# Optimization experiments

Hardware: AMD Instinct MI355X
Metric: run time of the kernel (lower is better)

Reference implementation:

```python
import jax, jax.numpy as jnp
import numpy as np

B, S, D = 8, 1024, 1024
H, K = 16, 64  # num_heads, key_dim
NEG_INF = -1e9  # Keras _large_compatible_negative for float32


def setup_inputs() -> dict:
    key = jax.random.key(0)
    ks = jax.random.split(key, 10)
    x = jax.random.normal(ks[0], (B, S, D), dtype=jnp.float32)
    mask = jax.random.bernoulli(ks[1], 0.9, (B, S))  # bool per-token mask
    w = lambda k, shp: (0.02 * jax.random.normal(k, shp, dtype=jnp.float32))
    return {
        "input_tensor": x,
        "input_mask": mask,
        "Wq": w(ks[2], (D, H, K)), "bq": jnp.zeros((H, K), jnp.float32),
        "Wk": w(ks[3], (D, H, K)), "bk": jnp.zeros((H, K), jnp.float32),
        "Wv": w(ks[4], (D, H, K)), "bv": jnp.zeros((H, K), jnp.float32),
        "Wo": w(ks[5], (H, K, D)), "bo": jnp.zeros((D,), jnp.float32),
    }


def reference(input_tensor, input_mask, Wq, bq, Wk, bk, Wv, bv, Wo, bo):
    x = input_tensor
    # QKV projections: [B,S,D] x [D,H,K] -> [B,S,H,K]
    q = jnp.einsum("bsd,dhk->bshk", x, Wq) + bq
    k = jnp.einsum("bsd,dhk->bshk", x, Wk) + bk
    v = jnp.einsum("bsd,dhk->bshk", x, Wv) + bv
    # scaled dot-product scores: [B,H,Sq,Sk]
    scores = jnp.einsum("bqhk,bshk->bhqs", q, k) / jnp.sqrt(
        jnp.asarray(K, x.dtype))
    # mask = logical_and(mask[...,None], mask[...,None,:]) per example
    m2 = (input_mask[:, :, None] & input_mask[:, None, :])  # [B,Sq,Sk]
    scores = scores + (1.0 - m2[:, None, :, :].astype(x.dtype)) * NEG_INF
    probs = jax.nn.softmax(scores, axis=-1)
    # attend and project out: [B,S,H,K] -> [B,S,D]
    ctx = jnp.einsum("bhqs,bshk->bqhk", probs, v)
    return jnp.einsum("bqhk,hkd->bqd", ctx, Wo) + bo
```

## Files before the change

kernel.cpp:

```cpp
#include <hip/hip_runtime.h>
#include <math.h>

#define Ss 1024
#define Dd 1024
#define Hh 16
#define Kk 64

typedef __bf16 bf16x8 __attribute__((ext_vector_type(8)));
typedef __bf16 bf16x4 __attribute__((ext_vector_type(4)));
typedef float  f32x4  __attribute__((ext_vector_type(4)));

#define MFMA16(a, b, c) __builtin_amdgcn_mfma_f32_16x16x32_bf16(a, b, c, 0, 0, 0)

#define XB_E   8388608u
#define WT_E   3145728u
#define WOT_E  1048576u
#define QKV_E  8388608u

#define QSC 0.18033688011112042f

__device__ __forceinline__ float exp2_hw(float x) {
    float r; asm("v_exp_f32 %0, %1" : "=v"(r) : "v"(x)); return r;
}

typedef __attribute__((address_space(1))) const void gas_void;
typedef __attribute__((address_space(3))) void las_void;
__device__ __forceinline__ void gll16(const __bf16* g, char* l) {
    __builtin_amdgcn_global_load_lds((gas_void*)g, (las_void*)l, 16, 0, 0);
}

__global__ __launch_bounds__(256) void prep(
    const float* __restrict__ x,
    const float* __restrict__ Wq, const float* __restrict__ Wk,
    const float* __restrict__ Wv, const float* __restrict__ Wo,
    __bf16* __restrict__ xb, __bf16* __restrict__ WT, __bf16* __restrict__ WoT)
{
    __shared__ float tile[64][65];
    const int z = blockIdx.z;
    const int t = threadIdx.x;

    if (z == 4) {
        size_t blk = blockIdx.y * 16 + blockIdx.x;
        const float4* src = (const float4*)(x + blk * 32768);
        bf16x4* dst = (bf16x4*)(((__bf16*)xb) + blk * 32768);
        #pragma unroll
        for (int u = 0; u < 32; ++u) {
            float4 v = src[u * 256 + t];
            dst[u * 256 + t] =
                (bf16x4){(__bf16)v.x, (__bf16)v.y, (__bf16)v.z, (__bf16)v.w};
        }
        return;
    }

    const float* src = (z == 0) ? Wq : (z == 1) ? Wk : (z == 2) ? Wv : Wo;
    __bf16* dst = (z < 3) ? (WT + (size_t)z * 1048576) : WoT;

    int r0 = blockIdx.y * 64, c0 = blockIdx.x * 64;
    int rr = t >> 2, cg = (t & 3) * 16;

    #pragma unroll
    for (int u = 0; u < 4; ++u) {
        float4 v = *(const float4*)(src + (size_t)(r0 + rr) * 1024 + c0 + cg + u * 4);
        tile[rr][cg + u * 4 + 0] = v.x;
        tile[rr][cg + u * 4 + 1] = v.y;
        tile[rr][cg + u * 4 + 2] = v.z;
        tile[rr][cg + u * 4 + 3] = v.w;
    }
    __syncthreads();
    bf16x8 o0, o1;
    #pragma unroll
    for (int jj = 0; jj < 8; ++jj) o0[jj] = (__bf16)tile[cg + jj][rr];
    #pragma unroll
    for (int jj = 0; jj < 8; ++jj) o1[jj] = (__bf16)tile[cg + 8 + jj][rr];
    __bf16* dp = dst + (size_t)(c0 + rr) * 1024 + r0 + cg;
    *(bf16x8*)dp = o0;
    *(bf16x8*)(dp + 8) = o1;
}

__global__ __launch_bounds__(512, 2) void gemm_qkv(
    const __bf16* __restrict__ A, const __bf16* __restrict__ Bt,
    __bf16* __restrict__ qb, __bf16* __restrict__ kb, __bf16* __restrict__ vb,
    const float* __restrict__ bq, const float* __restrict__ bk,
    const float* __restrict__ bv)
{
    __shared__ __align__(16) __bf16 As[2][256][64];
    __shared__ __align__(16) __bf16 Bs[2][256][64];

    const int t = threadIdx.x;
    const int wave = t >> 6, lane = t & 63;
    const int quad = lane >> 4, l16 = lane & 15;
    const int wm = wave >> 2, wn = wave & 3;

    const int nwg = gridDim.x * gridDim.y;
    const int cpx = nwg >> 3;
    int g = blockIdx.y * gridDim.x + blockIdx.x;
    g = (g & 7) * cpx + (g >> 3);
    const int bx = g % gridDim.x, by = g / gridDim.x;
    const int m0 = by * 256, n0 = bx * 256;

    const int srow = t >> 3;
    const int scol = (((t & 7) ^ (srow & 7)) * 8);
    const __bf16* pa = A  + (size_t)(m0 + srow) * 1024 + scol;
    const __bf16* pb = Bt + (size_t)(n0 + srow) * 1024 + scol;
    char* lA = (char*)(&As[0][0][0]) + t * 16;
    char* lB = (char*)(&Bs[0][0][0]) + t * 16;

#define STAGE(slot, k0) do {                                     \
        gll16(pa + (k0),           lA + (slot) * 32768);         \
        gll16(pa + (k0) +  65536,  lA + (slot) * 32768 +  8192); \
        gll16(pa + (k0) + 131072,  lA + (slot) * 32768 + 16384); \
        gll16(pa + (k0) + 196608,  lA + (slot) * 32768 + 24576); \
        gll16(pb + (k0),           lB + (slot) * 32768);         \
        gll16(pb + (k0) +  65536,  lB + (slot) * 32768 +  8192); \
        gll16(pb + (k0) + 131072,  lB + (slot) * 32768 + 16384); \
        gll16(pb + (k0) + 196608,  lB + (slot) * 32768 + 24576); \
    } while (0)

    STAGE(0, 0);
    STAGE(1, 64);

    f32x4 acc[8][4];
    #pragma unroll
    for (int i = 0; i < 8; ++i)
        #pragma unroll
        for (int j = 0; j < 4; ++j) acc[i][j] = (f32x4){0.f, 0.f, 0.f, 0.f};

    const int swz = (l16 & 7) << 4;

    for (int it = 0; it < 16; ++it) {
        const int s = it & 1;
        if (it == 15) asm volatile("s_waitcnt vmcnt(0)" ::: "memory");
        else          asm volatile("s_waitcnt vmcnt(8)" ::: "memory");
        __builtin_amdgcn_s_barrier();

        const char* baseA = (const char*)&As[s][0][0];
        const char* baseB = (const char*)&Bs[s][0][0];

        bf16x8 bfrag[2][4];
        #pragma unroll
        for (int nj = 0; nj < 4; ++nj) {
            int rowb = (wn * 64 + nj * 16 + l16) * 128;
            bfrag[0][nj] = *(const bf16x8*)(baseB + rowb + ((quad * 16) ^ swz));
            bfrag[1][nj] = *(const bf16x8*)(baseB + rowb + ((64 + quad * 16) ^ swz));
        }

        {
            bf16x8 afr[4][2];
            #pragma unroll
            for (int mi = 0; mi < 4; ++mi) {
                int rowa = (wm * 128 + mi * 16 + l16) * 128;
                afr[mi][0] = *(const bf16x8*)(baseA + rowa + ((quad * 16) ^ swz));
                afr[mi][1] = *(const bf16x8*)(baseA + rowa + ((64 + quad * 16) ^ swz));
            }
            __builtin_amdgcn_s_setprio(1);
            #pragma unroll
            for (int mi = 0; mi < 4; ++mi)
                #pragma unroll
                for (int nj = 0; nj < 4; ++nj)
                    acc[mi][nj] = MFMA16(afr[mi][1], bfrag[1][nj],
                                  MFMA16(afr[mi][0], bfrag[0][nj], acc[mi][nj]));
            __builtin_amdgcn_s_setprio(0);
        }
        __builtin_amdgcn_s_barrier();

        {
            bf16x8 afr[4][2];
            #pragma unroll
            for (int mi = 0; mi < 4; ++mi) {
                int rowa = (wm * 128 + (mi + 4) * 16 + l16) * 128;
                afr[mi][0] = *(const bf16x8*)(baseA + rowa + ((quad * 16) ^ swz));
                afr[mi][1] = *(const bf16x8*)(baseA + rowa + ((64 + quad * 16) ^ swz));
            }
            asm volatile("s_waitcnt lgkmcnt(0)" ::: "memory");
            __builtin_amdgcn_sched_barrier(0);
            __builtin_amdgcn_s_barrier();
            if (it < 14) STAGE(s, (it + 2) * 64);

            __builtin_amdgcn_s_setprio(1);
            #pragma unroll
            for (int mi = 0; mi < 4; ++mi)
                #pragma unroll
                for (int nj = 0; nj < 4; ++nj)
                    acc[mi + 4][nj] = MFMA16(afr[mi][1], bfrag[1][nj],
                                      MFMA16(afr[mi][0], bfrag[0][nj], acc[mi + 4][nj]));
            __builtin_amdgcn_s_setprio(0);
        }
    }
#undef STAGE

    {
        const int z = n0 >> 10;
        const float* bias = (z == 0) ? bq : (z == 1) ? bk : bv;
        const float sc2 = (z == 0) ? QSC : 1.0f;
        #pragma unroll
        for (int mi = 0; mi < 8; ++mi) {
            int row = m0 + wm * 128 + mi * 16 + quad * 4;
            int b = row >> 10, sx = row & 1023;
            #pragma unroll
            for (int nj = 0; nj < 4; ++nj) {
                int n1 = (n0 + wn * 64 + nj * 16 + l16) & 1023;
                int h = n1 >> 6, ch = n1 & 63;
                float bia = bias[n1];
                if (z < 2) {
                    __bf16* dst = ((z == 0) ? qb : kb)
                        + ((size_t)(b * Hh + h) * Ss + sx) * Kk + ch;
                    #pragma unroll
                    for (int r = 0; r < 4; ++r)
                        dst[(size_t)r * Kk] = (__bf16)((acc[mi][nj][r] + bia) * sc2);
                } else {
                    float bia2 = bv[n1];
                    bf16x4 o;
                    #pragma unroll
                    for (int r = 0; r < 4; ++r) o[r] = (__bf16)(acc[mi][nj][r] + bia2);
                    *(bf16x4*)(vb + ((size_t)(b * Hh + h) * Kk + ch) * Ss + sx) = o;
                }
            }
        }
    }
}

__global__ __launch_bounds__(512) void gemm_out(
    const __bf16* __restrict__ A, const __bf16* __restrict__ Bt,
    float* __restrict__ outf, const float* __restrict__ bo)
{
    __shared__ __align__(16) __bf16 As[2][256][64];
    __shared__ __align__(16) __bf16 Bs[2][128][64];

    const int t = threadIdx.x;
    const int wave = t >> 6, lane = t & 63;
    const int quad = lane >> 4, l16 = lane & 15;
    const int wm = wave >> 2, wn = wave & 3;

    const int nwg = gridDim.x * gridDim.y;
    const int cpx = nwg >> 3;
    int g = blockIdx.y * gridDim.x + blockIdx.x;
    g = (g & 7) * cpx + (g >> 3);
    const int bx = g % gridDim.x, by = g / gridDim.x;
    const int m0 = by * 256, n0 = bx * 128;

    const int srow = t >> 3;
    const int scol = (((t & 7) ^ (srow & 7)) * 8);
    const __bf16* pa = A  + (size_t)(m0 + srow) * 1024 + scol;
    const __bf16* pb = Bt + (size_t)(n0 + srow) * 1024 + scol;
    char* lA = (char*)(&As[0][0][0]) + t * 16;
    char* lB = (char*)(&Bs[0][0][0]) + t * 16;

#define SGA(slot, k0, c) gll16(pa + (k0) + (c) * 65536, lA + (slot) * 32768 + (c) * 8192)
#define SGB(slot, k0, c) gll16(pb + (k0) + (c) * 65536, lB + (slot) * 16384 + (c) * 8192)

    SGA(0, 0, 0); SGA(0, 0, 2);
    SGB(0, 0, 0); SGB(0, 0, 1);
    SGA(0, 0, 1); SGA(0, 0, 3);

    f32x4 acc[8][2];
    #pragma unroll
    for (int i = 0; i < 8; ++i)
        #pragma unroll
        for (int j = 0; j < 2; ++j) acc[i][j] = (f32x4){0.f, 0.f, 0.f, 0.f};

    const int swz = (l16 & 7) << 4;

    asm volatile("s_waitcnt vmcnt(2)" ::: "memory");
    __syncthreads();

    for (int it = 0; it < 16; ++it) {
        const int s = it & 1, ns = s ^ 1;
        const int kn = (it + 1) * 64;
        const bool st = (it < 15);
        const char* baseA = (const char*)&As[s][0][0];
        const char* baseB = (const char*)&Bs[s][0][0];

        bf16x8 af[4][2], b0f[2][2];

        asm volatile("s_waitcnt vmcnt(0)" ::: "memory");
        #pragma unroll
        for (int mi = 0; mi < 4; ++mi) {
            int ra = (wm * 128 + mi * 16 + l16) * 128;
            af[mi][0] = *(const bf16x8*)(baseA + ra + ((quad * 16) ^ swz));
            af[mi][1] = *(const bf16x8*)(baseA + ra + ((64 + quad * 16) ^ swz));
        }
        #pragma unroll
        for (int nj = 0; nj < 2; ++nj) {
            int rb = (wn * 32 + nj * 16 + l16) * 128;
            b0f[nj][0] = *(const bf16x8*)(baseB + rb + ((quad * 16) ^ swz));
            b0f[nj][1] = *(const bf16x8*)(baseB + rb + ((64 + quad * 16) ^ swz));
        }
        if (st) { SGA(ns, kn, 0); SGA(ns, kn, 2); SGB(ns, kn, 0); SGB(ns, kn, 1); }
        __builtin_amdgcn_s_barrier();
        asm volatile("s_waitcnt lgkmcnt(0)" ::: "memory");
        __builtin_amdgcn_sched_barrier(0);
        __builtin_amdgcn_s_setprio(1);
        #pragma unroll
        for (int mi = 0; mi < 4; ++mi)
            #pragma unroll
            for (int nj = 0; nj < 2; ++nj)
                acc[mi][nj] = MFMA16(af[mi][1], b0f[nj][1],
                              MFMA16(af[mi][0], b0f[nj][0], acc[mi][nj]));
        __builtin_amdgcn_s_setprio(0);
        __builtin_amdgcn_s_barrier();

        asm volatile("s_waitcnt vmcnt(0)" ::: "memory");
        #pragma unroll
        for (int mi = 0; mi < 4; ++mi) {
            int ra = (wm * 128 + (4 + mi) * 16 + l16) * 128;
            af[mi][0] = *(const bf16x8*)(baseA + ra + ((quad * 16) ^ swz));
            af[mi][1] = *(const bf16x8*)(baseA + ra + ((64 + quad * 16) ^ swz));
        }
        if (st) { SGA(ns, kn, 1); SGA(ns, kn, 3); }
        __builtin_amdgcn_s_barrier();
        asm volatile("s_waitcnt lgkmcnt(0)" ::: "memory");
        __builtin_amdgcn_sched_barrier(0);
        __builtin_amdgcn_s_setprio(1);
        #pragma unroll
        for (int mi = 0; mi < 4; ++mi)
            #pragma unroll
            for (int nj = 0; nj < 2; ++nj)
                acc[4 + mi][nj] = MFMA16(af[mi][1], b0f[nj][1],
                                  MFMA16(af[mi][0], b0f[nj][0], acc[4 + mi][nj]));
        __builtin_amdgcn_s_setprio(0);
        __builtin_amdgcn_s_barrier();
    }
#undef SGA
#undef SGB

    #pragma unroll
    for (int mi = 0; mi < 8; ++mi) {
        int row = m0 + wm * 128 + mi * 16 + quad * 4;
        #pragma unroll
        for (int nj = 0; nj < 2; ++nj) {
            int n = n0 + wn * 32 + nj * 16 + l16;
            float bia = bo[n];
            #pragma unroll
            for (int r = 0; r < 4; ++r)
                outf[(size_t)(row + r) * 1024 + n] = acc[mi][nj][r] + bia;
        }
    }
}

__global__ __launch_bounds__(256) void attn(
    const __bf16* __restrict__ qb, const __bf16* __restrict__ kb,
    const __bf16* __restrict__ vb, const int* __restrict__ mask,
    __bf16* __restrict__ ctx)
{
    const int id = blockIdx.y * gridDim.x + blockIdx.x;
    const int bh = (id & 7) * 16 + ((id >> 3) & 15);
    const int q0 = (id >> 7) * 128;
    const int b  = bh >> 4;
    const int h  = bh & 15;
    const size_t base = (size_t)bh * Ss * Kk;

    __shared__ __align__(16) __bf16 Qs[128][72];
    __shared__ __align__(16) __bf16 Ks[2][64][72];
    __shared__ __align__(16) __bf16 VTs[2][64][72];
    __shared__ __align__(16) __bf16 Ps[4][32][72];
    __shared__ float mkf[1024];

    const int t    = threadIdx.x;
    const int wave = t >> 6, lane = t & 63;
    const int quad = lane >> 4, l16 = lane & 15;
    const int qbase = wave * 32;

    #pragma unroll
    for (int p = 0; p < 4; ++p) {
        int idx = t + p * 256;
        int r = idx >> 3, gq = idx & 7;
        *(bf16x8*)&Qs[r][gq * 8] =
            *(const bf16x8*)(qb + base + (size_t)(q0 + r) * Kk + gq * 8);
    }
    {
        int4 mi = *(const int4*)(mask + b * Ss + t * 4);
        mkf[t * 4 + 0] = (float)mi.x;
        mkf[t * 4 + 1] = (float)mi.y;
        mkf[t * 4 + 2] = (float)mi.z;
        mkf[t * 4 + 3] = (float)mi.w;
    }

    const int r0 = t >> 3, c0 = (t & 7) * 8;
    bf16x8 kr0, kr1, vr0, vr1;
    kr0 = *(const bf16x8*)(kb + base + (size_t)(r0) * Kk + c0);
    kr1 = *(const bf16x8*)(kb + base + (size_t)(r0 + 32) * Kk + c0);
    vr0 = *(const bf16x8*)(vb + base + (size_t)(r0) * Ss + c0);
    vr1 = *(const bf16x8*)(vb + base + (size_t)(r0 + 32) * Ss + c0);

    __syncthreads();

    bf16x8 aq[2][2];
    #pragma unroll
    for (int rg = 0; rg < 2; ++rg) {
        aq[rg][0] = *(const bf16x8*)&Qs[qbase + rg * 16 + l16][quad * 8];
        aq[rg][1] = *(const bf16x8*)&Qs[qbase + rg * 16 + l16][32 + quad * 8];
    }
    float mqf[2][4], omqf[2][4];
    #pragma unroll
    for (int rg = 0; rg < 2; ++rg)
        #pragma unroll
        for (int i = 0; i < 4; ++i) {
            float m = mkf[q0 + qbase + rg * 16 + quad * 4 + i];
            mqf[rg][i] = m; omqf[rg][i] = 1.0f - m;
        }

    f32x4 O[2][4];
    float lsum[2][4];
    #pragma unroll
    for (int rg = 0; rg < 2; ++rg)
        #pragma unroll
        for (int nb = 0; nb < 4; ++nb) O[rg][nb] = (f32x4){0.f, 0.f, 0.f, 0.f};
    #pragma unroll
    for (int rg = 0; rg < 2; ++rg)
        #pragma unroll
        for (int i = 0; i < 4; ++i) lsum[rg][i] = 0.f;

    for (int kt = 0; kt < Ss; kt += 64) {
        const int p = (kt >> 6) & 1;
        *(bf16x8*)&Ks[p][r0][c0] = kr0;
        *(bf16x8*)&Ks[p][r0 + 32][c0] = kr1;
        *(bf16x8*)&VTs[p][r0][c0] = vr0;
        *(bf16x8*)&VTs[p][r0 + 32][c0] = vr1;
        __syncthreads();

        int ktn = kt + 64;
        if (ktn < Ss) {
            kr0 = *(const bf16x8*)(kb + base + (size_t)(ktn + r0) * Kk + c0);
            kr1 = *(const bf16x8*)(kb + base + (size_t)(ktn + r0 + 32) * Kk + c0);
            vr0 = *(const bf16x8*)(vb + base + (size_t)(r0) * Ss + ktn + c0);
            vr1 = *(const bf16x8*)(vb + base + (size_t)(r0 + 32) * Ss + ktn + c0);
        }

        float mkv[4];
        #pragma unroll
        for (int nb = 0; nb < 4; ++nb) mkv[nb] = mkf[kt + nb * 16 + l16];

        bf16x8 kb0[4], kb1[4];
        #pragma unroll
        for (int nb = 0; nb < 4; ++nb) {
            kb0[nb] = *(const bf16x8*)&Ks[p][nb * 16 + l16][quad * 8];
            kb1[nb] = *(const bf16x8*)&Ks[p][nb * 16 + l16][32 + quad * 8];
        }

        f32x4 s[2][4];
        __builtin_amdgcn_s_setprio(1);
        #pragma unroll
        for (int rg = 0; rg < 2; ++rg)
            #pragma unroll
            for (int nb = 0; nb < 4; ++nb) {
                f32x4 a = (f32x4){0.f, 0.f, 0.f, 0.f};
                a = MFMA16(aq[rg][0], kb0[nb], a);
                a = MFMA16(aq[rg][1], kb1[nb], a);
                s[rg][nb] = a;
            }
        __builtin_amdgcn_s_setprio(0);

        #pragma unroll
        for (int rg = 0; rg < 2; ++rg)
            #pragma unroll
            for (int i = 0; i < 4; ++i) {
                float ls = 0.f;
                #pragma unroll
                for (int nb = 0; nb < 4; ++nb) {
                    float pv = exp2_hw(s[rg][nb][i]) * mkv[nb];
                    pv = pv * mqf[rg][i] + omqf[rg][i];
                    Ps[wave][rg * 16 + quad * 4 + i][nb * 16 + l16] = (__bf16)pv;
                    ls += pv;
                }
                lsum[rg][i] += ls;
            }

        bf16x8 ap0[2], ap1[2];
        #pragma unroll
        for (int rg = 0; rg < 2; ++rg) {
            ap0[rg] = *(const bf16x8*)&Ps[wave][rg * 16 + l16][quad * 8];
            ap1[rg] = *(const bf16x8*)&Ps[wave][rg * 16 + l16][32 + quad * 8];
        }
        __builtin_amdgcn_s_setprio(1);
        #pragma unroll
        for (int nb = 0; nb < 4; ++nb) {
            bf16x8 vb0 = *(const bf16x8*)&VTs[p][nb * 16 + l16][quad * 8];
            bf16x8 vb1 = *(const bf16x8*)&VTs[p][nb * 16 + l16][32 + quad * 8];
            #pragma unroll
            for (int rg = 0; rg < 2; ++rg) {
                O[rg][nb] = MFMA16(ap0[rg], vb0, O[rg][nb]);
                O[rg][nb] = MFMA16(ap1[rg], vb1, O[rg][nb]);
            }
        }
        __builtin_amdgcn_s_setprio(0);
    }

    #pragma unroll
    for (int rg = 0; rg < 2; ++rg)
        #pragma unroll
        for (int i = 0; i < 4; ++i) {
            float l = lsum[rg][i];
            l += __shfl_xor(l, 1);
            l += __shfl_xor(l, 2);
            l += __shfl_xor(l, 4);
            l += __shfl_xor(l, 8);
            float inv = 1.0f / l;
            int srow = q0 + qbase + rg * 16 + quad * 4 + i;
            __bf16* dst = ctx + ((size_t)(b * Ss + srow) * Hh + h) * Kk;
            #pragma unroll
            for (int nb = 0; nb < 4; ++nb)
                dst[nb * 16 + l16] = (__bf16)(O[rg][nb][i] * inv);
        }
}

extern "C" void kernel_launch(void* const* d_in, const int* in_sizes, int n_in,
                              void* d_out, int out_size, void* d_ws, size_t ws_size,
                              hipStream_t stream) {
    const float* x    = (const float*)d_in[0];
    const int*   mask = (const int*)d_in[1];
    const float* Wq   = (const float*)d_in[2];
    const float* bq   = (const float*)d_in[3];
    const float* Wk   = (const float*)d_in[4];
    const float* bk   = (const float*)d_in[5];
    const float* Wv   = (const float*)d_in[6];
    const float* bv   = (const float*)d_in[7];
    const float* Wo   = (const float*)d_in[8];
    const float* bo   = (const float*)d_in[9];

    __bf16* xb   = (__bf16*)d_ws;
    __bf16* WT   = xb + XB_E;
    __bf16* WoT  = WT + WT_E;
    __bf16* qb   = WoT + WOT_E;
    __bf16* kb   = qb + QKV_E;
    __bf16* vb   = kb + QKV_E;
    __bf16* ctxb = vb + QKV_E;
    float* out = (float*)d_out;

    prep<<<dim3(16, 16, 5), 256, 0, stream>>>(x, Wq, Wk, Wv, Wo, xb, WT, WoT);
    gemm_qkv<<<dim3(12, 32), 512, 0, stream>>>(xb, WT, qb, kb, vb, bq, bk, bv);
    attn<<<dim3(128, 8), 256, 0, stream>>>(qb, kb, vb, mask, ctxb);
    gemm_out<<<dim3(8, 32), 512, 0, stream>>>(ctxb, WoT, out, bo);
}
```

Baseline: 259.8 us.

## Compute transposed scores and shuffle P in registers to drop LDS staging

The attention kernel now computes S^T (K as the A operand), so each lane holds one query row's scores. The probabilities are packed to bf16 with v_cvt_pk and rearranged into the PV MFMA operand with cross-lane shuffles, which removes the Ps shared-memory round trip. Q fragments are loaded straight from global memory, so the Qs tile is gone and LDS use drops, and launch bounds request 3 blocks per SIMD. The block index mapping is simplified and the output is written as vectorized bf16x4 stores. In exchange each tile now runs many shuffles, and the occupancy hint adds register pressure.

```diff
diff --git a/kernel.cpp b/kernel.cpp
--- a/kernel.cpp
+++ b/kernel.cpp
@@ -21,6 +21,11 @@
 
 __device__ __forceinline__ float exp2_hw(float x) {
     float r; asm("v_exp_f32 %0, %1" : "=v"(r) : "v"(x)); return r;
+}
+__device__ __forceinline__ unsigned cvtpk(float lo, float hi) {
+    unsigned r;
+    asm("v_cvt_pk_bf16_f32 %0, %1, %2" : "=v"(r) : "v"(lo), "v"(hi));
+    return r;
 }
 
 typedef __attribute__((address_space(1))) const void gas_void;
@@ -337,22 +342,19 @@
     }
 }
 
-__global__ __launch_bounds__(256) void attn(
+__global__ __launch_bounds__(256, 3) void attn(
     const __bf16* __restrict__ qb, const __bf16* __restrict__ kb,
     const __bf16* __restrict__ vb, const int* __restrict__ mask,
     __bf16* __restrict__ ctx)
 {
-    const int id = blockIdx.y * gridDim.x + blockIdx.x;
-    const int bh = (id & 7) * 16 + ((id >> 3) & 15);
-    const int q0 = (id >> 7) * 128;
+    const int bh = blockIdx.x;
+    const int q0 = blockIdx.y * 128;
     const int b  = bh >> 4;
     const int h  = bh & 15;
     const size_t base = (size_t)bh * Ss * Kk;
 
-    __shared__ __align__(16) __bf16 Qs[128][72];
     __shared__ __align__(16) __bf16 Ks[2][64][72];
     __shared__ __align__(16) __bf16 VTs[2][64][72];
-    __shared__ __align__(16) __bf16 Ps[4][32][72];
     __shared__ float mkf[1024];
 
     const int t    = threadIdx.x;
@@ -360,13 +362,6 @@
     const int quad = lane >> 4, l16 = lane & 15;
     const int qbase = wave * 32;
 
-    #pragma unroll
-    for (int p = 0; p < 4; ++p) {
-        int idx = t + p * 256;
-        int r = idx >> 3, gq = idx & 7;
-        *(bf16x8*)&Qs[r][gq * 8] =
-            *(const bf16x8*)(qb + base + (size_t)(q0 + r) * Kk + gq * 8);
-    }
     {
         int4 mi = *(const int4*)(mask + b * Ss + t * 4);
         mkf[t * 4 + 0] = (float)mi.x;
@@ -382,33 +377,33 @@
     vr0 = *(const bf16x8*)(vb + base + (size_t)(r0) * Ss + c0);
     vr1 = *(const bf16x8*)(vb + base + (size_t)(r0 + 32) * Ss + c0);
 
+    bf16x8 aq[2][2];
+    #pragma unroll
+    for (int rg = 0; rg < 2; ++rg) {
+        const __bf16* qrow = qb + base + (size_t)(q0 + qbase + rg * 16 + l16) * Kk;
+        aq[rg][0] = *(const bf16x8*)(qrow + quad * 8);
+        aq[rg][1] = *(const bf16x8*)(qrow + 32 + quad * 8);
+    }
+
     __syncthreads();
 
-    bf16x8 aq[2][2];
+    float mq[2], omq[2];
     #pragma unroll
     for (int rg = 0; rg < 2; ++rg) {
-        aq[rg][0] = *(const bf16x8*)&Qs[qbase + rg * 16 + l16][quad * 8];
-        aq[rg][1] = *(const bf16x8*)&Qs[qbase + rg * 16 + l16][32 + quad * 8];
-    }
-    float mqf[2][4], omqf[2][4];
+        float m_ = mkf[q0 + qbase + rg * 16 + l16];
+        mq[rg] = m_; omq[rg] = 1.0f - m_;
+    }
+
+    f32x4 O[2][4];
+    float lsum[2] = {0.f, 0.f};
     #pragma unroll
     for (int rg = 0; rg < 2; ++rg)
         #pragma unroll
-        for (int i = 0; i < 4; ++i) {
-            float m = mkf[q0 + qbase + rg * 16 + quad * 4 + i];
-            mqf[rg][i] = m; omqf[rg][i] = 1.0f - m;
-        }
-
-    f32x4 O[2][4];
-    float lsum[2][4];
-    #pragma unroll
-    for (int rg = 0; rg < 2; ++rg)
-        #pragma unroll
         for (int nb = 0; nb < 4; ++nb) O[rg][nb] = (f32x4){0.f, 0.f, 0.f, 0.f};
-    #pragma unroll
-    for (int rg = 0; rg < 2; ++rg)
-        #pragma unroll
-        for (int i = 0; i < 4; ++i) lsum[rg][i] = 0.f;
+
+    const int SA = ((quad & 1) << 5) | l16;
+    const int SB = SA + 16;
+    const bool hi = (quad >> 1) != 0;
 
     for (int kt = 0; kt < Ss; kt += 64) {
         const int p = (kt >> 6) & 1;
@@ -426,10 +421,6 @@
             vr1 = *(const bf16x8*)(vb + base + (size_t)(r0 + 32) * Ss + ktn + c0);
         }
 
-        float mkv[4];
-        #pragma unroll
-        for (int nb = 0; nb < 4; ++nb) mkv[nb] = mkf[kt + nb * 16 + l16];
-
         bf16x8 kb0[4], kb1[4];
         #pragma unroll
         for (int nb = 0; nb < 4; ++nb) {
@@ -444,63 +435,78 @@
             #pragma unroll
             for (int nb = 0; nb < 4; ++nb) {
                 f32x4 a = (f32x4){0.f, 0.f, 0.f, 0.f};
-                a = MFMA16(aq[rg][0], kb0[nb], a);
-                a = MFMA16(aq[rg][1], kb1[nb], a);
+                a = MFMA16(kb0[nb], aq[rg][0], a);
+                a = MFMA16(kb1[nb], aq[rg][1], a);
                 s[rg][nb] = a;
             }
         __builtin_amdgcn_s_setprio(0);
 
-        #pragma unroll
-        for (int rg = 0; rg < 2; ++rg)
-            #pragma unroll
-            for (int i = 0; i < 4; ++i) {
-                float ls = 0.f;
+        bf16x8 vbf0[4], vbf1[4];
+        #pragma unroll
+        for (int nb = 0; nb < 4; ++nb) {
+            vbf0[nb] = *(const bf16x8*)&VTs[p][nb * 16 + l16][quad * 8];
+            vbf1[nb] = *(const bf16x8*)&VTs[p][nb * 16 + l16][32 + quad * 8];
+        }
+
+        #pragma unroll
+        for (int rg = 0; rg < 2; ++rg) {
+            float ls = 0.f;
+            unsigned pk[4][2];
+            #pragma unroll
+            for (int nb = 0; nb < 4; ++nb) {
+                float4 mk4 = *(const float4*)&mkf[kt + nb * 16 + quad * 4];
                 #pragma unroll
-                for (int nb = 0; nb < 4; ++nb) {
-                    float pv = exp2_hw(s[rg][nb][i]) * mkv[nb];
-                    pv = pv * mqf[rg][i] + omqf[rg][i];
-                    Ps[wave][rg * 16 + quad * 4 + i][nb * 16 + l16] = (__bf16)pv;
+                for (int i = 0; i < 4; ++i) {
+                    float e = exp2_hw(s[rg][nb][i]);
+                    float pv = e * ((const float*)&mk4)[i] * mq[rg] + omq[rg];
+                    s[rg][nb][i] = pv;
                     ls += pv;
                 }
-                lsum[rg][i] += ls;
+                pk[nb][0] = cvtpk(s[rg][nb][0], s[rg][nb][1]);
+                pk[nb][1] = cvtpk(s[rg][nb][2], s[rg][nb][3]);
             }
-
-        bf16x8 ap0[2], ap1[2];
-        #pragma unroll
-        for (int rg = 0; rg < 2; ++rg) {
-            ap0[rg] = *(const bf16x8*)&Ps[wave][rg * 16 + l16][quad * 8];
-            ap1[rg] = *(const bf16x8*)&Ps[wave][rg * 16 + l16][32 + quad * 8];
-        }
-        __builtin_amdgcn_s_setprio(1);
+            lsum[rg] += ls;
+
+            #pragma unroll
+            for (int m = 0; m < 2; ++m) {
+                unsigned a0 = (unsigned)__shfl((int)pk[2 * m][0], SA);
+                unsigned b0 = (unsigned)__shfl((int)pk[2 * m + 1][0], SA);
+                unsigned a1 = (unsigned)__shfl((int)pk[2 * m][1], SA);
+                unsigned b1 = (unsigned)__shfl((int)pk[2 * m + 1][1], SA);
+                unsigned a2 = (unsigned)__shfl((int)pk[2 * m][0], SB);
+                unsigned b2 = (unsigned)__shfl((int)pk[2 * m + 1][0], SB);
+                unsigned a3 = (unsigned)__shfl((int)pk[2 * m][1], SB);
+                unsigned b3 = (unsigned)__shfl((int)pk[2 * m + 1][1], SB);
+                union { unsigned u[4]; bf16x8 v; } bb;
+                bb.u[0] = hi ? b0 : a0;
+                bb.u[1] = hi ? b1 : a1;
+                bb.u[2] = hi ? b2 : a2;
+                bb.u[3] = hi ? b3 : a3;
+                __builtin_amdgcn_s_setprio(1);
+                #pragma unroll
+                for (int nb = 0; nb < 4; ++nb)
+                    O[rg][nb] = MFMA16(m ? vbf1[nb] : vbf0[nb], bb.v, O[rg][nb]);
+                __builtin_amdgcn_s_setprio(0);
+            }
+        }
+    }
+
+    #pragma unroll
+    for (int rg = 0; rg < 2; ++rg) {
+        float l = lsum[rg];
+        l += __shfl_xor(l, 16);
+        l += __shfl_xor(l, 32);
+        float inv = 1.0f / l;
+        int srow = q0 + qbase + rg * 16 + l16;
+        __bf16* dst = ctx + ((size_t)(b * Ss + srow) * Hh + h) * Kk;
         #pragma unroll
         for (int nb = 0; nb < 4; ++nb) {
-            bf16x8 vb0 = *(const bf16x8*)&VTs[p][nb * 16 + l16][quad * 8];
-            bf16x8 vb1 = *(const bf16x8*)&VTs[p][nb * 16 + l16][32 + quad * 8];
-            #pragma unroll
-            for (int rg = 0; rg < 2; ++rg) {
-                O[rg][nb] = MFMA16(ap0[rg], vb0, O[rg][nb]);
-                O[rg][nb] = MFMA16(ap1[rg], vb1, O[rg][nb]);
-            }
-        }
-        __builtin_amdgcn_s_setprio(0);
-    }
-
-    #pragma unroll
-    for (int rg = 0; rg < 2; ++rg)
-        #pragma unroll
-        for (int i = 0; i < 4; ++i) {
-            float l = lsum[rg][i];
-            l += __shfl_xor(l, 1);
-            l += __shfl_xor(l, 2);
-            l += __shfl_xor(l, 4);
-            l += __shfl_xor(l, 8);
-            float inv = 1.0f / l;
-            int srow = q0 + qbase + rg * 16 + quad * 4 + i;
-            __bf16* dst = ctx + ((size_t)(b * Ss + srow) * Hh + h) * Kk;
-            #pragma unroll
-            for (int nb = 0; nb < 4; ++nb)
-                dst[nb * 16 + l16] = (__bf16)(O[rg][nb][i] * inv);
-        }
+            bf16x4 o;
+            #pragma unroll
+            for (int i = 0; i < 4; ++i) o[i] = (__bf16)(O[rg][nb][i] * inv);
+            *(bf16x4*)(dst + nb * 16 + quad * 4) = o;
+        }
+    }
 }
 
 extern "C" void kernel_launch(void* const* d_in, const int* in_sizes, int n_in,
```

Result: no change. 259.2 us (-0.3%).
